# Kernel optimization log

Hardware: AMD Instinct MI355X
Metric: run time of the kernel (lower is better)

The kernel has to match this reference:

```python
import jax, jax.numpy as jnp
import numpy as np

L, Q = 256, 21
LAMBDA_H = 1e-06
LAMBDA_J = 0.0001
M = 8192


def setup_inputs() -> dict:
    key = jax.random.key(0)
    k1, k2, k3, k4 = jax.random.split(key, 4)
    seqs = jax.random.randint(k1, (M, L), 0, Q, dtype=jnp.int64 if jax.config.jax_enable_x64 else jnp.int32)
    weights = jax.random.uniform(k2, (M,), dtype=jnp.float32)
    h = jax.random.normal(k3, (L, Q), dtype=jnp.float32) * 0.1
    J = jax.random.normal(k4, (L, L, Q, Q), dtype=jnp.float32) * 0.02
    return {"seqs": seqs, "weights": weights, "h": h, "J": J}


def reference(seqs, weights, h, J):
    # strictly-lower-triangular mask over (i, j): j < i
    tril = jnp.tril(jnp.ones((L, L), dtype=bool), k=-1)
    Jm = J * tril[:, :, None, None]                       # (L, L, q, q)

    # one-hot history; H[b, j, k] = 1 iff seqs[b, j] == k
    H = jax.nn.one_hot(seqs, Q, dtype=h.dtype)            # (M, L, q)

    # contrib[b, i, a] = sum_{j<i, k} J[i, j, a, k] * H[b, j, k]
    # == one big (M, L*q) x (L*q, L*q) causal-masked matmul
    contrib = jnp.einsum('ijak,bjk->bia', Jm, H)          # (M, L, q)

    logits = h[None, :, :] + contrib                      # (M, L, q)
    logp = jax.nn.log_softmax(logits, axis=-1)            # (M, L, q)

    # gather label log-probs
    ll = jnp.take_along_axis(logp, seqs[..., None], axis=-1)[..., 0]  # (M, L)

    M_eff = jnp.maximum(weights.sum(), 1e-12)
    w_norm = weights / M_eff
    nll = -(w_norm[:, None] * ll).sum()

    reg_h = 0.5 * LAMBDA_H * jnp.sum(h ** 2)
    reg_J = 0.5 * LAMBDA_J * jnp.sum(Jm ** 2)
    loss = nll + reg_h + reg_J
    return (loss, nll, reg_h + reg_J)
```

## Files before the change

### kernel.cpp

```cpp
#include <hip/hip_runtime.h>
#include <cstdint>
#include <cstddef>

#define L_   256
#define Q_   21
#define M_   8192
#define QQ   441
#define JCH  16
#define SCALE    32.0f
#define INVSCALE 0.03125f
#define NPAIR ((L_ * (L_ - 1)) / 2)


typedef _Float16 h2 __attribute__((ext_vector_type(2)));

__device__ __forceinline__ float block_reduce_sum(float v) {
    __shared__ float s[256];
    int t = threadIdx.x;
    __syncthreads();
    s[t] = v;
    __syncthreads();
#pragma unroll
    for (int o = 128; o > 0; o >>= 1) {
        if (t < o) s[t] += s[t + o];
        __syncthreads();
    }
    return s[0];
}

__global__ __launch_bounds__(256) void k_prep(const float* __restrict__ J,
                                              unsigned* __restrict__ Jt,
                                              float* __restrict__ acc) {
    __shared__ __align__(16) float sB[16 * QQ];
    const int t  = threadIdx.x;
    const int i  = blockIdx.y + 1;
    const int j0 = blockIdx.x << 4;
    if (j0 >= i) return;
    const int jn = min(16, i - j0);

    const size_t base_dw = (size_t)(i * L_ + j0) * QQ;
    const float* src = J + base_dw;
    const int ndw = jn * QQ;
    const int nf4 = ndw >> 2;
    const int rem = ndw & 3;

    float v2 = 0.f;
    {
        const float4* src4 = reinterpret_cast<const float4*>(src);
        float4* s4 = reinterpret_cast<float4*>(sB);
        for (int q = t; q < nf4; q += 256) {
            float4 v = src4[q];
            s4[q] = v;
            v2 += v.x * v.x + v.y * v.y + v.z * v.z + v.w * v.w;
        }
        if (t < rem) {
            float v = src[(nf4 << 2) + t];
            sB[(nf4 << 2) + t] = v;
            v2 += v * v;
        }
    }
    __syncthreads();

    {
        const int nu4 = jn << 6;
        uint4* dst = reinterpret_cast<uint4*>(Jt + (size_t)(i * L_ + j0) * 256);
        for (int g = t; g < nu4; g += 256) {
            const float* s = sB + (g >> 6) * QQ;
            unsigned wv[4];
#pragma unroll
            for (int c = 0; c < 4; ++c) {
                const int dd = ((g & 63) << 2) | c;
                const int kr = dd / 12;
                const int dw = dd - 12 * kr;
                const int a0 = dw << 1;
                unsigned outw = 0;
                if (kr < Q_) {
                    float x0 = (a0     < Q_) ? s[(a0    ) * Q_ + kr] : 0.f;
                    float x1 = (a0 + 1 < Q_) ? s[(a0 + 1) * Q_ + kr] : 0.f;
                    union { _Float16 hh[2]; unsigned u; } uu;
                    uu.hh[0] = (_Float16)(x0 * SCALE);
                    uu.hh[1] = (_Float16)(x1 * SCALE);
                    outw = uu.u;
                }
                wv[c] = outw;
            }
            uint4 o; o.x = wv[0]; o.y = wv[1]; o.z = wv[2]; o.w = wv[3];
            dst[g] = o;
        }
    }

    float r = block_reduce_sum(v2);
    if (t == 0) atomicAdd(&acc[4 + ((blockIdx.y * 16 + blockIdx.x) & 255)], r);
}

__global__ __launch_bounds__(256) void k_prep2(const int* __restrict__ seqs,
                                               const float* __restrict__ w,
                                               const float* __restrict__ h,
                                               unsigned* __restrict__ seqsP,
                                               float* __restrict__ acc) {
    const int bid = blockIdx.x;
    const int t = threadIdx.x;
    if (bid < 256) {
        const int bc = bid >> 3;
        const int jc = bid & 7;
        const int b = bc * 256 + t;
        const int4* row = reinterpret_cast<const int4*>(seqs + (size_t)b * L_);
#pragma unroll
        for (int u = 0; u < 8; ++u) {
            const int jq = jc * 8 + u;
            int4 v = row[jq];
            unsigned p = (unsigned)(v.x & 255) | ((unsigned)(v.y & 255) << 8) |
                         ((unsigned)(v.z & 255) << 16) | ((unsigned)(v.w & 255) << 24);
            seqsP[jq * M_ + b] = p;
        }
    } else if (bid == 256) {
        float v = 0.f;
        for (int x = t; x < M_; x += 256) v += w[x];
        float r = block_reduce_sum(v);
        if (t == 0) acc[0] = r;
    } else {
        float v2 = 0.f;
        for (int x = t; x < L_ * Q_; x += 256) { float y = h[x]; v2 += y * y; }
        float r2 = block_reduce_sum(v2);
        if (t == 0) acc[2] = r2;
    }
}

#define BODY(jj)                                                                    \
    {                                                                               \
        const unsigned kk = (idxw[(jj) >> 2] >> (((jj) & 3) * 8)) & 255u;           \
        const uint4* rp = reinterpret_cast<const uint4*>(sJ) + ((jj) * 64 + kk * 3);\
        union { uint4 u; h2 h[4]; } ra, rb, rc;                                     \
        ra.u = rp[0]; rb.u = rp[1]; rc.u = rp[2];                                   \
        acch[0]  += ra.h[0]; acch[1]  += ra.h[1];                                   \
        acch[2]  += ra.h[2]; acch[3]  += ra.h[3];                                   \
        acch[4]  += rb.h[0]; acch[5]  += rb.h[1];                                   \
        acch[6]  += rb.h[2]; acch[7]  += rb.h[3];                                   \
        acch[8]  += rc.h[0]; acch[9]  += rc.h[1];                                   \
        acch[10] += rc.h[2]; acch[11] += rc.h[3];                                   \
    }

__global__ __launch_bounds__(256, 8) void k_main(const unsigned* __restrict__ Jt,
                                                 const float* __restrict__ h,
                                                 const unsigned* __restrict__ seqsP,
                                                 const float* __restrict__ weights,
                                                 float* __restrict__ acc) {
    __shared__ unsigned sJ[JCH * 256];

    const int bid = blockIdx.x;
    const int i = (L_ - 1) - (bid >> 5);
    const int b = ((bid & 31) << 8) + threadIdx.x;

    h2 acch[12];
    const float* hp = h + i * Q_;
#pragma unroll
    for (int m = 0; m < 10; ++m) {
        acch[m].x = (_Float16)(hp[2 * m] * SCALE);
        acch[m].y = (_Float16)(hp[2 * m + 1] * SCALE);
    }
    acch[10].x = (_Float16)(hp[20] * SCALE); acch[10].y = (_Float16)0.f;
    acch[11].x = (_Float16)0.f;              acch[11].y = (_Float16)0.f;

    const unsigned* Jrow = Jt + (size_t)i * (256 * 256);

    const int nStages = i >> 4;
    const int rem     = i & 15;

    for (int s = 0; s < nStages; ++s) {
        const int j0 = s << 4;
        {
            const uint4* src = reinterpret_cast<const uint4*>(Jrow + j0 * 256);
            uint4* dst = reinterpret_cast<uint4*>(sJ);
#pragma unroll
            for (int n = 0; n < 4; ++n) {
                dst[n * 256 + threadIdx.x] = src[n * 256 + threadIdx.x];
            }
        }
        __syncthreads();

        unsigned idxw[JCH / 4];
#pragma unroll
        for (int q = 0; q < JCH / 4; ++q) {
            idxw[q] = seqsP[((j0 >> 2) + q) * M_ + b];
        }

#pragma unroll
        for (int jj = 0; jj < JCH; ++jj) BODY(jj);

        __syncthreads();
    }

    if (rem) {
        const int j0 = nStages << 4;
        {
            const uint4* src = reinterpret_cast<const uint4*>(Jrow + j0 * 256);
            uint4* dst = reinterpret_cast<uint4*>(sJ);
#pragma unroll
            for (int n = 0; n < 4; ++n) {
                dst[n * 256 + threadIdx.x] = src[n * 256 + threadIdx.x];
            }
        }
        __syncthreads();

        unsigned idxw[JCH / 4];
#pragma unroll
        for (int q = 0; q < JCH / 4; ++q) {
            idxw[q] = seqsP[((j0 >> 2) + q) * M_ + b];
        }

#pragma unroll
        for (int jj = 0; jj < JCH; ++jj) {
            if (jj >= rem) break;
            BODY(jj);
        }
    }

    float l[21];
#pragma unroll
    for (int m = 0; m < 10; ++m) {
        l[2 * m]     = (float)acch[m].x * INVSCALE;
        l[2 * m + 1] = (float)acch[m].y * INVSCALE;
    }
    l[20] = (float)acch[10].x * INVSCALE;

    unsigned lw = seqsP[(i >> 2) * M_ + b];
    int lbl = (int)((lw >> ((i & 3) * 8)) & 255u);

    float m = l[0];
#pragma unroll
    for (int a = 1; a < 21; ++a) m = fmaxf(m, l[a]);
    float s = 0.f;
    float lv = l[0];
#pragma unroll
    for (int a = 0; a < 21; ++a) {
        s += __expf(l[a] - m);
        if (a > 0) lv = (a == lbl) ? l[a] : lv;
    }
    float ll = (lv - m) - __logf(s);
    float contrib = weights[b] * ll;

    float r = block_reduce_sum(contrib);
    if (threadIdx.x == 0) atomicAdd(&acc[260 + (bid & 127)], r);
}

__global__ void k_final(const float* __restrict__ acc, float* __restrict__ out) {
    int t = threadIdx.x;
    float j2p = acc[4 + t];
    float j2 = block_reduce_sum(j2p);
    float llp = (t < 128) ? acc[260 + t] : 0.f;
    float lls = block_reduce_sum(llp);
    if (t == 0) {
        float wsum = fmaxf(acc[0], 1e-12f);
        float nll = -lls / wsum;
        float reg = 0.5e-6f * acc[2] + 0.5e-4f * j2;
        out[0] = nll + reg;
        out[1] = nll;
        out[2] = reg;
    }
}

extern "C" void kernel_launch(void* const* d_in, const int* in_sizes, int n_in,
                              void* d_out, int out_size, void* d_ws, size_t ws_size,
                              hipStream_t stream) {
    const int*   seqs    = (const int*)d_in[0];
    const float* weights = (const float*)d_in[1];
    const float* h       = (const float*)d_in[2];
    const float* J       = (const float*)d_in[3];
    float* out = (float*)d_out;

    char* ws = (char*)d_ws;
    float*    acc   = (float*)ws;
    unsigned* seqsP = (unsigned*)(ws + 2048);
    unsigned* Jt    = (unsigned*)(ws + 2048 + (size_t)(L_ / 4) * M_ * sizeof(unsigned));

    hipMemsetAsync(d_ws, 0, 2048, stream);

    dim3 pg(16, 255);
    k_prep<<<pg, 256, 0, stream>>>(J, Jt, acc);
    k_prep2<<<258, 256, 0, stream>>>(seqs, weights, h, seqsP, acc);
    k_main<<<L_ * (M_ / 256), 256, 0, stream>>>(Jt, h, seqsP, weights, acc);
    k_final<<<1, 256, 0, stream>>>(acc, out);
}
```

Baseline: 391.9 us.

## Fuse prep, main and final kernels into one cooperative persistent kernel

Replaces the four-kernel sequence with a single cooperative launch that does J conversion, sequence packing and reductions, then a grid sync, the main per-position log-likelihood loop, another grid sync and the final combine. Jt is stored in packed triangular layout instead of a full L×L grid. Reductions go through spread atomics into per-slot accumulators. This removes launch gaps and shrinks the Jt footprint, at the cost of grid-wide barriers and a persistent-loop schedule. A fallback path keeps the old multi-kernel sequence.

```diff
diff --git a/kernel.cpp b/kernel.cpp
--- a/kernel.cpp
+++ b/kernel.cpp
@@ -1,4 +1,5 @@
 #include <hip/hip_runtime.h>
+#include <hip/hip_cooperative_groups.h>
 #include <cstdint>
 #include <cstddef>
 
@@ -26,6 +27,227 @@
         __syncthreads();
     }
     return s[0];
+}
+
+#define BODY(jj)                                                                    \
+    {                                                                               \
+        const unsigned kk = (idxw[(jj) >> 2] >> (((jj) & 3) * 8)) & 255u;           \
+        const uint4* rp = reinterpret_cast<const uint4*>(sJ) + ((jj) * 64 + kk * 3);\
+        union { uint4 u; h2 h[4]; } ra, rb, rc;                                     \
+        ra.u = rp[0]; rb.u = rp[1]; rc.u = rp[2];                                   \
+        acch[0]  += ra.h[0]; acch[1]  += ra.h[1];                                   \
+        acch[2]  += ra.h[2]; acch[3]  += ra.h[3];                                   \
+        acch[4]  += rb.h[0]; acch[5]  += rb.h[1];                                   \
+        acch[6]  += rb.h[2]; acch[7]  += rb.h[3];                                   \
+        acch[8]  += rc.h[0]; acch[9]  += rc.h[1];                                   \
+        acch[10] += rc.h[2]; acch[11] += rc.h[3];                                   \
+    }
+
+__global__ __launch_bounds__(256, 8) void k_all(
+        const int* __restrict__ seqs, const float* __restrict__ w,
+        const float* __restrict__ hvec, const float* __restrict__ J,
+        unsigned* __restrict__ seqsP, unsigned* __restrict__ Jt,
+        float* __restrict__ acc, float* __restrict__ out) {
+    __shared__ __align__(16) unsigned sJ[JCH * 256];
+    const int t   = threadIdx.x;
+    const int bid = blockIdx.x;
+    const int gsz = gridDim.x;
+
+    float v2acc = 0.f;
+    for (int c = bid; c < 8418; c += gsz) {
+        if (c < 8160) {
+            const int i  = (c >> 5) + 1;
+            const int j0 = (c & 31) << 3;
+            if (j0 >= i) continue;
+            const int jn = (i - j0 < 8) ? (i - j0) : 8;
+            float* sB = reinterpret_cast<float*>(sJ);
+            const float* src = J + (size_t)(i * L_ + j0) * QQ;
+            const int ndw = jn * QQ;
+            const int nf4 = ndw >> 2;
+            const int rem = ndw & 3;
+            __syncthreads();
+            {
+                const float4* src4 = reinterpret_cast<const float4*>(src);
+                float4* s4 = reinterpret_cast<float4*>(sB);
+                for (int q = t; q < nf4; q += 256) {
+                    float4 v = src4[q];
+                    s4[q] = v;
+                    v2acc += v.x * v.x + v.y * v.y + v.z * v.z + v.w * v.w;
+                }
+                if (t < rem) {
+                    float v = src[(nf4 << 2) + t];
+                    sB[(nf4 << 2) + t] = v;
+                    v2acc += v * v;
+                }
+            }
+            __syncthreads();
+            {
+                const int tri = i * (i - 1) / 2;
+                uint4* dst = reinterpret_cast<uint4*>(Jt + (size_t)(tri + j0) * 256);
+                const int nu4 = jn << 6;
+                for (int gq = t; gq < nu4; gq += 256) {
+                    const float* s = sB + (gq >> 6) * QQ;
+                    unsigned wv[4];
+#pragma unroll
+                    for (int c4 = 0; c4 < 4; ++c4) {
+                        const int dd = ((gq & 63) << 2) | c4;
+                        const int kr = dd / 12;
+                        const int dw = dd - 12 * kr;
+                        const int a0 = dw << 1;
+                        unsigned outw = 0;
+                        if (kr < Q_) {
+                            float x0 = (a0     < Q_) ? s[(a0    ) * Q_ + kr] : 0.f;
+                            float x1 = (a0 + 1 < Q_) ? s[(a0 + 1) * Q_ + kr] : 0.f;
+                            union { _Float16 hh[2]; unsigned u; } uu;
+                            uu.hh[0] = (_Float16)(x0 * SCALE);
+                            uu.hh[1] = (_Float16)(x1 * SCALE);
+                            outw = uu.u;
+                        }
+                        wv[c4] = outw;
+                    }
+                    uint4 o; o.x = wv[0]; o.y = wv[1]; o.z = wv[2]; o.w = wv[3];
+                    dst[gq] = o;
+                }
+            }
+        } else if (c < 8416) {
+            const int u  = c - 8160;
+            const int b  = ((u >> 3) << 8) + t;
+            const int jc = u & 7;
+            const int4* row = reinterpret_cast<const int4*>(seqs + (size_t)b * L_);
+#pragma unroll
+            for (int u8 = 0; u8 < 8; ++u8) {
+                const int jq = jc * 8 + u8;
+                int4 v = row[jq];
+                unsigned p = (unsigned)(v.x & 255) | ((unsigned)(v.y & 255) << 8) |
+                             ((unsigned)(v.z & 255) << 16) | ((unsigned)(v.w & 255) << 24);
+                seqsP[jq * M_ + b] = p;
+            }
+        } else if (c == 8416) {
+            float v = 0.f;
+            for (int x = t; x < M_; x += 256) v += w[x];
+            float r = block_reduce_sum(v);
+            if (t == 0) acc[0] = r;
+        } else {
+            float v2 = 0.f;
+            for (int x = t; x < L_ * Q_; x += 256) { float y = hvec[x]; v2 += y * y; }
+            float r2 = block_reduce_sum(v2);
+            if (t == 0) acc[2] = r2;
+        }
+    }
+    {
+        float r = block_reduce_sum(v2acc);
+        if (t == 0) atomicAdd(&acc[4 + (bid & 255)], r);
+    }
+
+    cooperative_groups::this_grid().sync();
+
+    for (int n = bid; n < 8192; n += gsz) {
+        const int i = (L_ - 1) - (n >> 5);
+        const int b = ((n & 31) << 8) + t;
+
+        h2 acch[12];
+        const float* hp = hvec + i * Q_;
+#pragma unroll
+        for (int m = 0; m < 10; ++m) {
+            acch[m].x = (_Float16)(hp[2 * m] * SCALE);
+            acch[m].y = (_Float16)(hp[2 * m + 1] * SCALE);
+        }
+        acch[10].x = (_Float16)(hp[20] * SCALE); acch[10].y = (_Float16)0.f;
+        acch[11].x = (_Float16)0.f;              acch[11].y = (_Float16)0.f;
+
+        const unsigned* Jrow = Jt + (size_t)(i * (i - 1) / 2) * 256;
+        const int nStages = i >> 4;
+        const int rem     = i & 15;
+
+        for (int s = 0; s < nStages; ++s) {
+            const int j0 = s << 4;
+            __syncthreads();
+            {
+                const uint4* src = reinterpret_cast<const uint4*>(Jrow + j0 * 256);
+                uint4* dst = reinterpret_cast<uint4*>(sJ);
+#pragma unroll
+                for (int nq = 0; nq < 4; ++nq)
+                    dst[nq * 256 + t] = src[nq * 256 + t];
+            }
+            __syncthreads();
+
+            unsigned idxw[JCH / 4];
+#pragma unroll
+            for (int q = 0; q < JCH / 4; ++q)
+                idxw[q] = seqsP[((j0 >> 2) + q) * M_ + b];
+
+#pragma unroll
+            for (int jj = 0; jj < JCH; ++jj) BODY(jj);
+        }
+
+        if (rem) {
+            const int j0 = nStages << 4;
+            __syncthreads();
+            {
+                const uint4* src = reinterpret_cast<const uint4*>(Jrow + j0 * 256);
+                uint4* dst = reinterpret_cast<uint4*>(sJ);
+#pragma unroll
+                for (int nq = 0; nq < 4; ++nq)
+                    dst[nq * 256 + t] = src[nq * 256 + t];
+            }
+            __syncthreads();
+
+            unsigned idxw[JCH / 4];
+#pragma unroll
+            for (int q = 0; q < JCH / 4; ++q)
+                idxw[q] = seqsP[((j0 >> 2) + q) * M_ + b];
+
+#pragma unroll
+            for (int jj = 0; jj < JCH; ++jj) {
+                if (jj >= rem) break;
+                BODY(jj);
+            }
+        }
+
+        float l[21];
+#pragma unroll
+        for (int m = 0; m < 10; ++m) {
+            l[2 * m]     = (float)acch[m].x * INVSCALE;
+            l[2 * m + 1] = (float)acch[m].y * INVSCALE;
+        }
+        l[20] = (float)acch[10].x * INVSCALE;
+
+        unsigned lw = seqsP[(i >> 2) * M_ + b];
+        int lbl = (int)((lw >> ((i & 3) * 8)) & 255u);
+
+        float m = l[0];
+#pragma unroll
+        for (int a = 1; a < 21; ++a) m = fmaxf(m, l[a]);
+        float sx = 0.f;
+        float lv = l[0];
+#pragma unroll
+        for (int a = 0; a < 21; ++a) {
+            sx += __expf(l[a] - m);
+            if (a > 0) lv = (a == lbl) ? l[a] : lv;
+        }
+        float ll = (lv - m) - __logf(sx);
+        float contrib = w[b] * ll;
+
+        float r = block_reduce_sum(contrib);
+        if (t == 0) atomicAdd(&acc[260 + (n & 127)], r);
+    }
+
+    cooperative_groups::this_grid().sync();
+
+    if (bid == 0) {
+        float j2p = acc[4 + t];
+        float j2 = block_reduce_sum(j2p);
+        float llp = (t < 128) ? acc[260 + t] : 0.f;
+        float lls = block_reduce_sum(llp);
+        if (t == 0) {
+            float wsum = fmaxf(acc[0], 1e-12f);
+            float nll = -lls / wsum;
+            float reg = 0.5e-6f * acc[2] + 0.5e-4f * j2;
+            out[0] = nll + reg;
+            out[1] = nll;
+            out[2] = reg;
+        }
+    }
 }
 
 __global__ __launch_bounds__(256) void k_prep(const float* __restrict__ J,
@@ -38,8 +260,7 @@
     if (j0 >= i) return;
     const int jn = min(16, i - j0);
 
-    const size_t base_dw = (size_t)(i * L_ + j0) * QQ;
-    const float* src = J + base_dw;
+    const float* src = J + (size_t)(i * L_ + j0) * QQ;
     const int ndw = jn * QQ;
     const int nf4 = ndw >> 2;
     const int rem = ndw & 3;
@@ -62,8 +283,9 @@
     __syncthreads();
 
     {
+        const int tri = i * (i - 1) / 2;
         const int nu4 = jn << 6;
-        uint4* dst = reinterpret_cast<uint4*>(Jt + (size_t)(i * L_ + j0) * 256);
+        uint4* dst = reinterpret_cast<uint4*>(Jt + (size_t)(tri + j0) * 256);
         for (int g = t; g < nu4; g += 256) {
             const float* s = sB + (g >> 6) * QQ;
             unsigned wv[4];
@@ -126,25 +348,11 @@
     }
 }
 
-#define BODY(jj)                                                                    \
-    {                                                                               \
-        const unsigned kk = (idxw[(jj) >> 2] >> (((jj) & 3) * 8)) & 255u;           \
-        const uint4* rp = reinterpret_cast<const uint4*>(sJ) + ((jj) * 64 + kk * 3);\
-        union { uint4 u; h2 h[4]; } ra, rb, rc;                                     \
-        ra.u = rp[0]; rb.u = rp[1]; rc.u = rp[2];                                   \
-        acch[0]  += ra.h[0]; acch[1]  += ra.h[1];                                   \
-        acch[2]  += ra.h[2]; acch[3]  += ra.h[3];                                   \
-        acch[4]  += rb.h[0]; acch[5]  += rb.h[1];                                   \
-        acch[6]  += rb.h[2]; acch[7]  += rb.h[3];                                   \
-        acch[8]  += rc.h[0]; acch[9]  += rc.h[1];                                   \
-        acch[10] += rc.h[2]; acch[11] += rc.h[3];                                   \
-    }
-
-__global__ __launch_bounds__(256, 8) void k_main(const unsigned* __restrict__ Jt,
-                                                 const float* __restrict__ h,
-                                                 const unsigned* __restrict__ seqsP,
-                                                 const float* __restrict__ weights,
-                                                 float* __restrict__ acc) {
+__global__ __launch_bounds__(256, 8) void k_main_fb(const unsigned* __restrict__ Jt,
+                                                    const float* __restrict__ h,
+                                                    const unsigned* __restrict__ seqsP,
+                                                    const float* __restrict__ weights,
+                                                    float* __restrict__ acc) {
     __shared__ unsigned sJ[JCH * 256];
 
     const int bid = blockIdx.x;
@@ -161,52 +369,47 @@
     acch[10].x = (_Float16)(hp[20] * SCALE); acch[10].y = (_Float16)0.f;
     acch[11].x = (_Float16)0.f;              acch[11].y = (_Float16)0.f;
 
-    const unsigned* Jrow = Jt + (size_t)i * (256 * 256);
-
+    const unsigned* Jrow = Jt + (size_t)(i * (i - 1) / 2) * 256;
     const int nStages = i >> 4;
     const int rem     = i & 15;
 
     for (int s = 0; s < nStages; ++s) {
         const int j0 = s << 4;
+        __syncthreads();
         {
             const uint4* src = reinterpret_cast<const uint4*>(Jrow + j0 * 256);
             uint4* dst = reinterpret_cast<uint4*>(sJ);
 #pragma unroll
-            for (int n = 0; n < 4; ++n) {
+            for (int n = 0; n < 4; ++n)
                 dst[n * 256 + threadIdx.x] = src[n * 256 + threadIdx.x];
-            }
         }
         __syncthreads();
 
         unsigned idxw[JCH / 4];
 #pragma unroll
-        for (int q = 0; q < JCH / 4; ++q) {
+        for (int q = 0; q < JCH / 4; ++q)
             idxw[q] = seqsP[((j0 >> 2) + q) * M_ + b];
-        }
 
 #pragma unroll
         for (int jj = 0; jj < JCH; ++jj) BODY(jj);
-
-        __syncthreads();
     }
 
     if (rem) {
         const int j0 = nStages << 4;
+        __syncthreads();
         {
             const uint4* src = reinterpret_cast<const uint4*>(Jrow + j0 * 256);
             uint4* dst = reinterpret_cast<uint4*>(sJ);
 #pragma unroll
-            for (int n = 0; n < 4; ++n) {
+            for (int n = 0; n < 4; ++n)
                 dst[n * 256 + threadIdx.x] = src[n * 256 + threadIdx.x];
-            }
         }
         __syncthreads();
 
         unsigned idxw[JCH / 4];
 #pragma unroll
-        for (int q = 0; q < JCH / 4; ++q) {
+        for (int q = 0; q < JCH / 4; ++q)
             idxw[q] = seqsP[((j0 >> 2) + q) * M_ + b];
-        }
 
 #pragma unroll
         for (int jj = 0; jj < JCH; ++jj) {
@@ -275,9 +478,37 @@
 
     hipMemsetAsync(d_ws, 0, 2048, stream);
 
-    dim3 pg(16, 255);
-    k_prep<<<pg, 256, 0, stream>>>(J, Jt, acc);
-    k_prep2<<<258, 256, 0, stream>>>(seqs, weights, h, seqsP, acc);
-    k_main<<<L_ * (M_ / 256), 256, 0, stream>>>(Jt, h, seqsP, weights, acc);
-    k_final<<<1, 256, 0, stream>>>(acc, out);
-}
+    static int coopGrid = -1;
+    if (coopGrid < 0) {
+        int nb = 0;
+        if (hipOccupancyMaxActiveBlocksPerMultiprocessor(&nb, k_all, 256, 0) != hipSuccess)
+            nb = 0;
+        int dev = 0, cus = 0;
+        hipGetDevice(&dev);
+        if (hipDeviceGetAttribute(&cus, hipDeviceAttributeMultiprocessorCount, dev) != hipSuccess)
+            cus = 0;
+        long g = (long)nb * (long)cus;
+        coopGrid = (g >= 2048) ? 2048 : (int)g;
+    }
+
+    bool done = false;
+    if (coopGrid >= 256) {
+        const int*   a0 = seqs;  const float* a1 = weights;
+        const float* a2 = h;     const float* a3 = J;
+        unsigned*    a4 = seqsP; unsigned*    a5 = Jt;
+        float*       a6 = acc;   float*       a7 = out;
+        void* args[8] = {&a0, &a1, &a2, &a3, &a4, &a5, &a6, &a7};
+        hipError_t e = hipLaunchCooperativeKernel(k_all, dim3((unsigned)coopGrid),
+                                                  dim3(256), args, 0u, stream);
+        done = (e == hipSuccess);
+        if (!done) coopGrid = 0;
+    }
+
+    if (!done) {
+        dim3 pg(16, 255);
+        k_prep<<<pg, 256, 0, stream>>>(J, Jt, acc);
+        k_prep2<<<258, 256, 0, stream>>>(seqs, weights, h, seqsP, acc);
+        k_main_fb<<<L_ * (M_ / 256), 256, 0, stream>>>(Jt, h, seqsP, weights, acc);
+        k_final<<<1, 256, 0, stream>>>(acc, out);
+    }
+}
```

After: 674.2 us. 1.72x slower.

## Merge prep kernels, pack Jt triangularly, drop memset and atomics

Applied to the files above, without the earlier changes.

Folds the two preparation kernels into one launch, with block ranges assigned to J conversion, sequence packing and scalar reductions. The transposed half-precision J is now stored in a packed lower-triangular layout, so the workspace holds only the needed pairs. J is read and written with nontemporal loads and stores. Atomic accumulation into a memset workspace is replaced by per-block partial slots that the final kernel sums, which removes the memset launch and atomic contention but makes the final reduction read more values.

```diff
diff --git a/kernel.cpp b/kernel.cpp
--- a/kernel.cpp
+++ b/kernel.cpp
@@ -12,7 +12,12 @@
 #define NPAIR ((L_ * (L_ - 1)) / 2)
 
 
+#define NPREPT 4080
+#define GPREP  (NPREPT + 256 + 2)
+
 typedef _Float16 h2 __attribute__((ext_vector_type(2)));
+typedef float    f32x4 __attribute__((ext_vector_type(4)));
+typedef unsigned u32x4 __attribute__((ext_vector_type(4)));
 
 __device__ __forceinline__ float block_reduce_sum(float v) {
     __shared__ float s[256];
@@ -29,100 +34,103 @@
 }
 
 __global__ __launch_bounds__(256) void k_prep(const float* __restrict__ J,
+                                              const int* __restrict__ seqs,
+                                              const float* __restrict__ w,
+                                              const float* __restrict__ h,
                                               unsigned* __restrict__ Jt,
-                                              float* __restrict__ acc) {
-    __shared__ __align__(16) float sB[16 * QQ];
-    const int t  = threadIdx.x;
-    const int i  = blockIdx.y + 1;
-    const int j0 = blockIdx.x << 4;
-    if (j0 >= i) return;
-    const int jn = min(16, i - j0);
-
-    const size_t base_dw = (size_t)(i * L_ + j0) * QQ;
-    const float* src = J + base_dw;
-    const int ndw = jn * QQ;
-    const int nf4 = ndw >> 2;
-    const int rem = ndw & 3;
-
-    float v2 = 0.f;
-    {
-        const float4* src4 = reinterpret_cast<const float4*>(src);
-        float4* s4 = reinterpret_cast<float4*>(sB);
-        for (int q = t; q < nf4; q += 256) {
-            float4 v = src4[q];
-            s4[q] = v;
-            v2 += v.x * v.x + v.y * v.y + v.z * v.z + v.w * v.w;
-        }
-        if (t < rem) {
-            float v = src[(nf4 << 2) + t];
-            sB[(nf4 << 2) + t] = v;
-            v2 += v * v;
-        }
-    }
-    __syncthreads();
-
-    {
-        const int nu4 = jn << 6;
-        uint4* dst = reinterpret_cast<uint4*>(Jt + (size_t)(i * L_ + j0) * 256);
-        for (int g = t; g < nu4; g += 256) {
-            const float* s = sB + (g >> 6) * QQ;
-            unsigned wv[4];
-#pragma unroll
-            for (int c = 0; c < 4; ++c) {
-                const int dd = ((g & 63) << 2) | c;
-                const int kr = dd / 12;
-                const int dw = dd - 12 * kr;
-                const int a0 = dw << 1;
-                unsigned outw = 0;
-                if (kr < Q_) {
-                    float x0 = (a0     < Q_) ? s[(a0    ) * Q_ + kr] : 0.f;
-                    float x1 = (a0 + 1 < Q_) ? s[(a0 + 1) * Q_ + kr] : 0.f;
-                    union { _Float16 hh[2]; unsigned u; } uu;
-                    uu.hh[0] = (_Float16)(x0 * SCALE);
-                    uu.hh[1] = (_Float16)(x1 * SCALE);
-                    outw = uu.u;
-                }
-                wv[c] = outw;
-            }
-            uint4 o; o.x = wv[0]; o.y = wv[1]; o.z = wv[2]; o.w = wv[3];
-            dst[g] = o;
-        }
-    }
-
-    float r = block_reduce_sum(v2);
-    if (t == 0) atomicAdd(&acc[4 + ((blockIdx.y * 16 + blockIdx.x) & 255)], r);
-}
-
-__global__ __launch_bounds__(256) void k_prep2(const int* __restrict__ seqs,
-                                               const float* __restrict__ w,
-                                               const float* __restrict__ h,
-                                               unsigned* __restrict__ seqsP,
-                                               float* __restrict__ acc) {
+                                              unsigned* __restrict__ seqsP,
+                                              float* __restrict__ acc2,
+                                              float* __restrict__ scal) {
     const int bid = blockIdx.x;
     const int t = threadIdx.x;
-    if (bid < 256) {
-        const int bc = bid >> 3;
-        const int jc = bid & 7;
-        const int b = bc * 256 + t;
+
+    if (bid < NPREPT) {
+        __shared__ __align__(16) float sB[16 * QQ];
+        const int i  = (bid >> 4) + 1;
+        const int j0 = (bid & 15) << 4;
+        if (j0 >= i) {
+            if (t == 0) acc2[bid] = 0.f;
+            return;
+        }
+        const int jn = min(16, i - j0);
+
+        const float* src = J + (size_t)(i * L_ + j0) * QQ;
+        const int ndw = jn * QQ;
+        const int nf4 = ndw >> 2;
+        const int rem = ndw & 3;
+
+        float v2 = 0.f;
+        {
+            const f32x4* src4 = reinterpret_cast<const f32x4*>(src);
+            f32x4* s4 = reinterpret_cast<f32x4*>(sB);
+            for (int q = t; q < nf4; q += 256) {
+                f32x4 v = __builtin_nontemporal_load(src4 + q);
+                s4[q] = v;
+                v2 += v.x * v.x + v.y * v.y + v.z * v.z + v.w * v.w;
+            }
+            if (t < rem) {
+                float v = src[(nf4 << 2) + t];
+                sB[(nf4 << 2) + t] = v;
+                v2 += v * v;
+            }
+        }
+        __syncthreads();
+
+        {
+            const int tri = i * (i - 1) / 2;
+            const int nu4 = jn << 6;
+            u32x4* dst = reinterpret_cast<u32x4*>(Jt + (size_t)(tri + j0) * 256);
+            for (int g = t; g < nu4; g += 256) {
+                const float* s = sB + (g >> 6) * QQ;
+                unsigned wv[4];
+#pragma unroll
+                for (int c = 0; c < 4; ++c) {
+                    const int dd = ((g & 63) << 2) | c;
+                    const int kr = dd / 12;
+                    const int dw = dd - 12 * kr;
+                    const int a0 = dw << 1;
+                    unsigned outw = 0;
+                    if (kr < Q_) {
+                        float x0 = (a0     < Q_) ? s[(a0    ) * Q_ + kr] : 0.f;
+                        float x1 = (a0 + 1 < Q_) ? s[(a0 + 1) * Q_ + kr] : 0.f;
+                        union { _Float16 hh[2]; unsigned u; } uu;
+                        uu.hh[0] = (_Float16)(x0 * SCALE);
+                        uu.hh[1] = (_Float16)(x1 * SCALE);
+                        outw = uu.u;
+                    }
+                    wv[c] = outw;
+                }
+                u32x4 o;
+                o.x = wv[0]; o.y = wv[1]; o.z = wv[2]; o.w = wv[3];
+                __builtin_nontemporal_store(o, dst + g);
+            }
+        }
+
+        float r = block_reduce_sum(v2);
+        if (t == 0) acc2[bid] = r;
+    } else if (bid < NPREPT + 256) {
+        const int u  = bid - NPREPT;
+        const int b  = ((u >> 3) << 8) + t;
+        const int jc = u & 7;
         const int4* row = reinterpret_cast<const int4*>(seqs + (size_t)b * L_);
 #pragma unroll
-        for (int u = 0; u < 8; ++u) {
-            const int jq = jc * 8 + u;
+        for (int u8 = 0; u8 < 8; ++u8) {
+            const int jq = jc * 8 + u8;
             int4 v = row[jq];
             unsigned p = (unsigned)(v.x & 255) | ((unsigned)(v.y & 255) << 8) |
                          ((unsigned)(v.z & 255) << 16) | ((unsigned)(v.w & 255) << 24);
             seqsP[jq * M_ + b] = p;
         }
-    } else if (bid == 256) {
+    } else if (bid == NPREPT + 256) {
         float v = 0.f;
         for (int x = t; x < M_; x += 256) v += w[x];
         float r = block_reduce_sum(v);
-        if (t == 0) acc[0] = r;
+        if (t == 0) scal[0] = r;
     } else {
         float v2 = 0.f;
         for (int x = t; x < L_ * Q_; x += 256) { float y = h[x]; v2 += y * y; }
         float r2 = block_reduce_sum(v2);
-        if (t == 0) acc[2] = r2;
+        if (t == 0) scal[1] = r2;
     }
 }
 
@@ -144,7 +152,7 @@
                                                  const float* __restrict__ h,
                                                  const unsigned* __restrict__ seqsP,
                                                  const float* __restrict__ weights,
-                                                 float* __restrict__ acc) {
+                                                 float* __restrict__ accL) {
     __shared__ unsigned sJ[JCH * 256];
 
     const int bid = blockIdx.x;
@@ -161,8 +169,7 @@
     acch[10].x = (_Float16)(hp[20] * SCALE); acch[10].y = (_Float16)0.f;
     acch[11].x = (_Float16)0.f;              acch[11].y = (_Float16)0.f;
 
-    const unsigned* Jrow = Jt + (size_t)i * (256 * 256);
-
+    const unsigned* Jrow = Jt + (size_t)(i * (i - 1) / 2) * 256;
     const int nStages = i >> 4;
     const int rem     = i & 15;
 
@@ -240,19 +247,24 @@
     float contrib = weights[b] * ll;
 
     float r = block_reduce_sum(contrib);
-    if (threadIdx.x == 0) atomicAdd(&acc[260 + (bid & 127)], r);
-}
-
-__global__ void k_final(const float* __restrict__ acc, float* __restrict__ out) {
+    if (threadIdx.x == 0) accL[bid] = r;
+}
+
+__global__ __launch_bounds__(256) void k_final(const float* __restrict__ acc2,
+                                               const float* __restrict__ accL,
+                                               const float* __restrict__ scal,
+                                               float* __restrict__ out) {
     int t = threadIdx.x;
-    float j2p = acc[4 + t];
-    float j2 = block_reduce_sum(j2p);
-    float llp = (t < 128) ? acc[260 + t] : 0.f;
-    float lls = block_reduce_sum(llp);
+    float j2 = 0.f;
+    for (int x = t; x < NPREPT; x += 256) j2 += acc2[x];
+    j2 = block_reduce_sum(j2);
+    float lls = 0.f;
+    for (int x = t; x < M_; x += 256) lls += accL[x];
+    lls = block_reduce_sum(lls);
     if (t == 0) {
-        float wsum = fmaxf(acc[0], 1e-12f);
+        float wsum = fmaxf(scal[0], 1e-12f);
         float nll = -lls / wsum;
-        float reg = 0.5e-6f * acc[2] + 0.5e-4f * j2;
+        float reg = 0.5e-6f * scal[1] + 0.5e-4f * j2;
         out[0] = nll + reg;
         out[1] = nll;
         out[2] = reg;
@@ -269,15 +281,14 @@
     float* out = (float*)d_out;
 
     char* ws = (char*)d_ws;
-    float*    acc   = (float*)ws;
-    unsigned* seqsP = (unsigned*)(ws + 2048);
-    unsigned* Jt    = (unsigned*)(ws + 2048 + (size_t)(L_ / 4) * M_ * sizeof(unsigned));
-
-    hipMemsetAsync(d_ws, 0, 2048, stream);
-
-    dim3 pg(16, 255);
-    k_prep<<<pg, 256, 0, stream>>>(J, Jt, acc);
-    k_prep2<<<258, 256, 0, stream>>>(seqs, weights, h, seqsP, acc);
-    k_main<<<L_ * (M_ / 256), 256, 0, stream>>>(Jt, h, seqsP, weights, acc);
-    k_final<<<1, 256, 0, stream>>>(acc, out);
-}
+    float*    acc2  = (float*)ws;
+    float*    accL  = (float*)(ws + 16384);
+    float*    scal  = (float*)(ws + 49152);
+    unsigned* seqsP = (unsigned*)(ws + 65536);
+    unsigned* Jt    = (unsigned*)(ws + 65536 + (size_t)(L_ / 4) * M_ * sizeof(unsigned));
+
+
+    k_prep<<<GPREP, 256, 0, stream>>>(J, seqs, weights, h, Jt, seqsP, acc2, scal);
+    k_main<<<L_ * (M_ / 256), 256, 0, stream>>>(Jt, h, seqsP, weights, accL);
+    k_final<<<1, 256, 0, stream>>>(acc2, accL, scal, out);
+}
```

Result: no change. 387.6 us (-1.1%).
